# Performance work log

Measured on AMD Instinct MI355X. Metric: run time of the kernel, lower is better.

The kernel has to match this reference:

```python
import jax, jax.numpy as jnp
import numpy as np

T, H, NH, NKV, HD = 4096, 2048, 16, 2, 256
ROT = 64           # partial_rotary_factor 0.25 * head_dim 256
HALF = ROT // 2    # 32 == sum(mrope_section [11, 11, 10])
BASE = 10_000_000.0
EPS = 1e-6
SCALE = HD ** -0.5


def setup_inputs() -> dict:
    key = jax.random.key(0)
    ks = jax.random.split(key, 8)
    s = 0.02
    return {
        "positions": jnp.sort(jax.random.randint(ks[0], (3, T), 0, 4096), axis=-1),
        "hidden": jax.random.normal(ks[1], (T, H), jnp.float32),
        "Wq": jax.random.normal(ks[2], (H, NH * HD * 2), jnp.float32) * s,
        "Wk": jax.random.normal(ks[3], (H, NKV * HD), jnp.float32) * s,
        "Wv": jax.random.normal(ks[4], (H, NKV * HD), jnp.float32) * s,
        "Wo": jax.random.normal(ks[5], (NH * HD, H), jnp.float32) * s,
        "q_norm_w": jax.random.normal(ks[6], (HD,), jnp.float32) * 0.1,
        "k_norm_w": jax.random.normal(ks[7], (HD,), jnp.float32) * 0.1,
    }


def _rms(x, w):
    # GemmaRMSNorm: x / rms * (1 + w), per-head over last dim
    var = jnp.mean(x * x, axis=-1, keepdims=True)
    return x * jax.lax.rsqrt(var + EPS) * (1.0 + w)


def _rope_tables(positions):
    # interleaved MRoPE: freq j uses position axis j % 3 -> counts [11,11,10]
    inv_freq = BASE ** (-jnp.arange(0, ROT, 2, dtype=jnp.float32) / ROT)  # [HALF]
    axis = jnp.arange(HALF) % 3
    pos = positions[axis, :].astype(jnp.float32)   # [HALF, T]
    freqs = pos.T * inv_freq                       # [T, HALF]
    return jnp.cos(freqs), jnp.sin(freqs)


def _apply_rope(x, cos, sin):
    # x: [T, heads, HD]; rotate first ROT dims (neox half-split), rest pass through
    x1, x2 = x[..., :HALF], x[..., HALF:ROT]
    c, s = cos[:, None, :], sin[:, None, :]
    return jnp.concatenate([x1 * c - x2 * s, x2 * c + x1 * s, x[..., ROT:]], axis=-1)


def reference(positions, hidden, Wq, Wk, Wv, Wo, q_norm_w, k_norm_w):
    qg = (hidden @ Wq).reshape(T, NH, 2 * HD)
    q, gate = qg[..., :HD], qg[..., HD:]          # chunk(2, dim=-1)
    k = (hidden @ Wk).reshape(T, NKV, HD)
    v = (hidden @ Wv).reshape(T, NKV, HD)
    q = _rms(q, q_norm_w)
    k = _rms(k, k_norm_w)
    cos, sin = _rope_tables(positions)
    q = _apply_rope(q, cos, sin)
    k = _apply_rope(k, cos, sin)
    # GQA causal attention: group 16 Q heads over 2 KV heads
    g = NH // NKV
    q4 = q.reshape(T, NKV, g, HD)
    scores = jnp.einsum('qkgd,tkd->kgqt', q4, k) * SCALE   # [NKV, g, T, T]
    mask = jnp.tril(jnp.ones((T, T), dtype=bool))
    scores = jnp.where(mask[None, None], scores, -jnp.inf)
    probs = jax.nn.softmax(scores, axis=-1)
    o = jnp.einsum('kgqt,tkd->qkgd', probs, v).reshape(T, NH, HD)
    o = o * jax.nn.sigmoid(gate)                   # per-head output gating
    return o.reshape(T, NH * HD) @ Wo
```

## Files before the change

kernel.cpp:

```cpp
#include <hip/hip_runtime.h>
#include <hip/hip_bf16.h>


#define T_SZ 4096
#define H_SZ 2048
#define NH_SZ 16
#define NKV_SZ 2
#define HD_SZ 256
#define ATT_SCALE 0.0625f
#define SOFT_M 18.0f
#define EPS_ 1e-6f

typedef __attribute__((ext_vector_type(8))) short bf16x8;
typedef __attribute__((ext_vector_type(4))) float f32x4;

#define MFMA16(a, b, c) __builtin_amdgcn_mfma_f32_16x16x32_bf16((a), (b), (c), 0, 0, 0)

__device__ __forceinline__ void async16(const void* g, void* l) {
  __builtin_amdgcn_global_load_lds((const __attribute__((address_space(1))) void*)g,
                                   (__attribute__((address_space(3))) void*)l,
                                   16, 0, 0);
}

__device__ __forceinline__ float to_f(float x) { return x; }
__device__ __forceinline__ float to_f(__hip_bfloat16 x) { return __bfloat162float(x); }

union BfBits { __hip_bfloat16 h; unsigned short u; };

__device__ __forceinline__ unsigned short bf16_bits(__hip_bfloat16 h) {
  BfBits t; t.h = h; return t.u;
}

__device__ __forceinline__ unsigned pack_hilo(float v) {
  __hip_bfloat16 hi = __float2bfloat16(v);
  float rem = v - __bfloat162float(hi);
  __hip_bfloat16 lo = __float2bfloat16(rem);
  return (unsigned)bf16_bits(hi) | ((unsigned)bf16_bits(lo) << 16);
}

__global__ __launch_bounds__(256) void cast_f32_bf16(const float* __restrict__ in,
                                                     __hip_bfloat16* __restrict__ out,
                                                     int n4) {
  int i = blockIdx.x * 256 + threadIdx.x;
  if (i >= n4) return;
  float4 v = ((const float4*)in)[i];
  union { __hip_bfloat16 h[4]; uint2 u; } t;
  t.h[0] = __float2bfloat16(v.x);
  t.h[1] = __float2bfloat16(v.y);
  t.h[2] = __float2bfloat16(v.z);
  t.h[3] = __float2bfloat16(v.w);
  ((uint2*)out)[i] = t.u;
}

template <typename TIN>
__global__ __launch_bounds__(256) void transpose_cast(const TIN* __restrict__ in,
                                                      __hip_bfloat16* __restrict__ out,
                                                      int R, int C) {
  __shared__ TIN tile[32][33];
  int c0 = blockIdx.x * 32, r0 = blockIdx.y * 32;
  int tx = threadIdx.x & 31, ty = threadIdx.x >> 5;
#pragma unroll
  for (int i = 0; i < 32; i += 8)
    tile[ty + i][tx] = in[(long)(r0 + ty + i) * C + c0 + tx];
  __syncthreads();
#pragma unroll
  for (int i = 0; i < 32; i += 8)
    out[(long)(c0 + ty + i) * R + r0 + tx] = __float2bfloat16(to_f(tile[tx][ty + i]));
}

__global__ __launch_bounds__(512) void gemm_qg2(const __hip_bfloat16* __restrict__ A,
                                                const __hip_bfloat16* __restrict__ BT,
                                                float* __restrict__ qout,
                                                __hip_bfloat16* __restrict__ gate) {
  __shared__ __align__(16) __hip_bfloat16 As[4][8192];
  __shared__ __align__(16) __hip_bfloat16 Bs[4][8192];
  const int tid = threadIdx.x, wid = tid >> 6, lane = tid & 63;
  const int lo = lane & 15, quad = lane >> 4;
  const int wm = (wid >> 2) * 128, wn = (wid & 3) * 64;
  const int wg = blockIdx.x + blockIdx.y * 8;
  const int xcd = wg & 7, i_ = wg >> 3;
  const long n0 = (long)(xcd * 4 + (i_ & 3)) * 256;
  const long m0 = (long)(i_ >> 2) * 256;
  const int K = 2048;

  const int r0_ = tid >> 2;
  const int kc0 = (tid & 3) ^ ((tid >> 3) & 3);
  const __hip_bfloat16* sA0 = A + (m0 + r0_) * K + kc0 * 8;
  const __hip_bfloat16* sA1 = A + (m0 + r0_ + 128) * K + kc0 * 8;
  const __hip_bfloat16* sB0 = BT + (n0 + r0_) * K + kc0 * 8;
  const __hip_bfloat16* sB1 = BT + (n0 + r0_ + 128) * K + kc0 * 8;

  const int xq = (lo >> 1) & 3;
  const int aoff = (wm + lo) * 32 + ((quad ^ xq) * 8);
  const int boff = (wn + lo) * 32 + ((quad ^ xq) * 8);

  const f32x4 z4 = {0.f, 0.f, 0.f, 0.f};
  f32x4 acc[8][4];
#pragma unroll
  for (int fr = 0; fr < 8; ++fr)
#pragma unroll
    for (int fn = 0; fn < 4; ++fn) acc[fr][fn] = z4;

#define QG_STAGE(buf, kt) do {                                   \
    const int off_ = (kt) * 32;                                  \
    async16(sA0 + off_, &As[buf][tid * 8]);                      \
    async16(sA1 + off_, &As[buf][tid * 8 + 4096]);               \
    async16(sB0 + off_, &Bs[buf][tid * 8]);                      \
    async16(sB1 + off_, &Bs[buf][tid * 8 + 4096]);               \
  } while (0)

#define QG_COMPUTE(buf_) do {                                    \
    bf16x8 af[8], bq[4];                                         \
    _Pragma("unroll")                                            \
    for (int fr = 0; fr < 8; ++fr)                               \
      af[fr] = *(const bf16x8*)(&As[buf_][aoff + fr * 512]);     \
    _Pragma("unroll")                                            \
    for (int fn = 0; fn < 4; ++fn)                               \
      bq[fn] = *(const bf16x8*)(&Bs[buf_][boff + fn * 512]);     \
    __builtin_amdgcn_s_setprio(1);                               \
    _Pragma("unroll")                                            \
    for (int fr = 0; fr < 8; ++fr)                               \
      _Pragma("unroll")                                          \
      for (int fn = 0; fn < 4; ++fn)                             \
        acc[fr][fn] = MFMA16(af[fr], bq[fn], acc[fr][fn]);       \
    __builtin_amdgcn_s_setprio(0);                               \
  } while (0)

  QG_STAGE(0, 0); QG_STAGE(1, 1); QG_STAGE(2, 2);
  for (int kt = 0; kt < 61; ++kt) {
    asm volatile("s_waitcnt vmcnt(8)" ::: "memory");
    __builtin_amdgcn_s_barrier();
    __builtin_amdgcn_sched_barrier(0);
    QG_STAGE((kt + 3) & 3, kt + 3);
    __builtin_amdgcn_sched_barrier(0);
    QG_COMPUTE(kt & 3);
  }
  asm volatile("s_waitcnt vmcnt(8)" ::: "memory");
  __builtin_amdgcn_s_barrier();
  __builtin_amdgcn_sched_barrier(0);
  QG_COMPUTE(1);
  asm volatile("s_waitcnt vmcnt(4)" ::: "memory");
  __builtin_amdgcn_s_barrier();
  __builtin_amdgcn_sched_barrier(0);
  QG_COMPUTE(2);
  asm volatile("s_waitcnt vmcnt(0)" ::: "memory");
  __builtin_amdgcn_s_barrier();
  __builtin_amdgcn_sched_barrier(0);
  QG_COMPUTE(3);
#undef QG_STAGE
#undef QG_COMPUTE

#pragma unroll
  for (int fr = 0; fr < 8; ++fr)
#pragma unroll
    for (int fn = 0; fn < 4; ++fn)
#pragma unroll
      for (int rr = 0; rr < 4; ++rr) {
        long row = m0 + wm + fr * 16 + quad * 4 + rr;
        long col = n0 + wn + fn * 16 + lo;
        int head = (int)(col >> 9), c = (int)(col & 511);
        float v = acc[fr][fn][rr];
        if (c < 256)
          qout[(row * NH_SZ + head) * 256 + c] = v;
        else
          gate[(row * NH_SZ + head) * 256 + (c - 256)] = __float2bfloat16(v);
      }
}

__global__ __launch_bounds__(256) void gemm_kv(const __hip_bfloat16* __restrict__ A,
                                               const __hip_bfloat16* __restrict__ BT,
                                               float* __restrict__ kf,
                                               __hip_bfloat16* __restrict__ vraw,
                                               int M, int N, int K) {
  __shared__ __align__(16) __hip_bfloat16 As[128 * 32];
  __shared__ __align__(16) __hip_bfloat16 Bs[128 * 32];
  const int tid = threadIdx.x;
  const int wid = tid >> 6, lane = tid & 63;
  const int lo = lane & 15, quad = lane >> 4;
  const int wq = blockIdx.x + blockIdx.y * 8;
  const int xcd = wq & 7, idx = wq >> 3;
  const long n0 = (long)xcd * 128;
  const long m0 = (long)idx * 128;
  const int wm = (wid >> 1) * 64, wn = (wid & 1) * 64;
  const f32x4 z4 = {0.f, 0.f, 0.f, 0.f};
  f32x4 acc[4][4];
#pragma unroll
  for (int i = 0; i < 4; ++i)
#pragma unroll
    for (int j = 0; j < 4; ++j) acc[i][j] = z4;

  const int cf0 = tid, cf1 = 256 + tid;
  const int r0_ = cf0 >> 2, c0_ = (cf0 & 3) * 8;
  const int r1_ = cf1 >> 2, c1_ = (cf1 & 3) * 8;
  const __hip_bfloat16* a0 = A + (m0 + r0_) * K + c0_;
  const __hip_bfloat16* a1 = A + (m0 + r1_) * K + c1_;
  const __hip_bfloat16* b0 = BT + (n0 + r0_) * K + c0_;
  const __hip_bfloat16* b1 = BT + (n0 + r1_) * K + c1_;

  for (int k0 = 0; k0 < K; k0 += 32) {
    async16(a0 + k0, As + cf0 * 8);
    async16(a1 + k0, As + cf1 * 8);
    async16(b0 + k0, Bs + cf0 * 8);
    async16(b1 + k0, Bs + cf1 * 8);
    __syncthreads();
    bf16x8 af[4], bfv[4];
#pragma unroll
    for (int i = 0; i < 4; ++i)
      af[i] = *(const bf16x8*)(As + (wm + i * 16 + lo) * 32 + quad * 8);
#pragma unroll
    for (int i = 0; i < 4; ++i)
      bfv[i] = *(const bf16x8*)(Bs + (wn + i * 16 + lo) * 32 + quad * 8);
#pragma unroll
    for (int i = 0; i < 4; ++i)
#pragma unroll
      for (int j = 0; j < 4; ++j) acc[i][j] = MFMA16(af[i], bfv[j], acc[i][j]);
    __syncthreads();
  }
#pragma unroll
  for (int i = 0; i < 4; ++i)
#pragma unroll
    for (int j = 0; j < 4; ++j)
#pragma unroll
      for (int r = 0; r < 4; ++r) {
        long row = m0 + wm + i * 16 + quad * 4 + r;
        long col = n0 + wn + j * 16 + lo;
        float v = acc[i][j][r];
        if (col < 512)
          kf[row * 512 + col] = v;
        else
          vraw[row * 512 + (col - 512)] = __float2bfloat16(v);
      }
}

__global__ __launch_bounds__(256) void v_swizzle(const __hip_bfloat16* __restrict__ vraw,
                                                 __hip_bfloat16* __restrict__ vsw) {
  const int ktt = blockIdx.x, kvh = blockIdx.y, tid = threadIdx.x;
  __shared__ __hip_bfloat16 L[64 * 264];
#pragma unroll
  for (int it = 0; it < 8; ++it) {
    int cf = it * 256 + tid;
    int kv = cf >> 5, d0 = (cf & 31) * 8;
    *(uint4*)&L[kv * 264 + d0] =
        *(const uint4*)&vraw[(((long)ktt * 64 + kv) * NKV_SZ + kvh) * 256 + d0];
  }
  __syncthreads();
#pragma unroll
  for (int it = 0; it < 8; ++it) {
    int cf = it * 256 + tid;
    int c = cf >> 8, d = cf & 255;
    union { __hip_bfloat16 h[8]; uint4 u; } t;
#pragma unroll
    for (int e = 0; e < 8; ++e) t.h[e] = L[(c * 8 + e) * 264 + d];
    *(uint4*)&vsw[((long)kvh * 64 + ktt) * 16384 + (long)(c * 256 + d) * 8] = t.u;
  }
}

__global__ __launch_bounds__(256) void norm_rope_wave(float* __restrict__ qbuf,
                                                      const float* __restrict__ kbuf,
                                                      __hip_bfloat16* __restrict__ ksw,
                                                      const int* __restrict__ pos,
                                                      const float* __restrict__ qw,
                                                      const float* __restrict__ kw) {
  const int id = blockIdx.x * 4 + (threadIdx.x >> 6);
  const int lane = threadIdx.x & 63;
  const int h = id % 18, t = id / 18;
  const bool isq = h < NH_SZ;
  const float* ptr = isq ? qbuf + ((long)t * NH_SZ + h) * 256
                         : kbuf + ((long)t * NKV_SZ + (h - NH_SZ)) * 256;
  const float* w = isq ? qw : kw;
  float4 v = *(const float4*)(ptr + lane * 4);
  float4 wv = *(const float4*)(w + lane * 4);
  float s2 = v.x * v.x + v.y * v.y + v.z * v.z + v.w * v.w;
#pragma unroll
  for (int o = 32; o > 0; o >>= 1) s2 += __shfl_xor(s2, o);
  float sc = rsqrtf(s2 * (1.0f / 256.0f) + EPS_);
  float n[4];
  n[0] = v.x * sc * (1.0f + wv.x);
  n[1] = v.y * sc * (1.0f + wv.y);
  n[2] = v.z * sc * (1.0f + wv.z);
  n[3] = v.w * sc * (1.0f + wv.w);
  float pr[4];
#pragma unroll
  for (int j = 0; j < 4; ++j) pr[j] = __shfl_xor(n[j], 8);
  float o4[4];
  if (lane < 16) {
    int base_i = (lane & 7) * 4;
#pragma unroll
    for (int j = 0; j < 4; ++j) {
      int i = base_i + j;
      float p = (float)pos[(i % 3) * T_SZ + t];
      float fr = p * exp2f((float)i * (-0.72667177075661f));
      float c, s;
      sincosf(fr, &s, &c);
      o4[j] = (lane < 8) ? n[j] * c - pr[j] * s : n[j] * c + pr[j] * s;
    }
  } else {
#pragma unroll
    for (int j = 0; j < 4; ++j) o4[j] = n[j];
  }
  if (isq) {
    uint4 u;
    u.x = pack_hilo(o4[0]); u.y = pack_hilo(o4[1]);
    u.z = pack_hilo(o4[2]); u.w = pack_hilo(o4[3]);
    *(uint4*)((unsigned*)qbuf + ((long)t * NH_SZ + h) * 256 + lane * 4) = u;
  } else {
    int kv = h - NH_SZ;
    long tt = t >> 5; int r = t & 31;
    int c = lane >> 1, e0 = (lane & 1) * 4;
    union { __hip_bfloat16 h4[4]; uint2 u; } kk;
#pragma unroll
    for (int j = 0; j < 4; ++j) kk.h4[j] = __float2bfloat16(o4[j]);
    *(uint2*)&ksw[(((long)kv * 128 + tt) * 32 + c) * 256 + r * 8 + e0] = kk.u;
  }
}

__global__ __launch_bounds__(256) void attn_kernel(unsigned* __restrict__ Qp,
                                                   const __hip_bfloat16* __restrict__ Ksw,
                                                   const __hip_bfloat16* __restrict__ Vsw,
                                                   const __hip_bfloat16* __restrict__ Gt) {
  const int w = blockIdx.x + blockIdx.y * 64;
  const int xcd = w & 7, j = w >> 3;
  const int h = xcd * 2 + (j & 1);
  const int qt = 63 - (j >> 1);
  const int kvh = h >> 3;
  const int tid = threadIdx.x, wid = tid >> 6, lane = tid & 63;
  const int lo = lane & 15, quad = lane >> 4;
  __shared__ __align__(16) __hip_bfloat16 Ks[32 * 256];
  __shared__ __align__(16) __hip_bfloat16 Vs[4 * 2048];
  __shared__ __align__(16) __hip_bfloat16 Ps[4][16 * 40];

  __hip_bfloat16* myP = &Ps[wid][0];
  const f32x4 z4 = {0.f, 0.f, 0.f, 0.f};
  const int nt = 2 * (qt + 1);

  bf16x8 qh[8], ql[8];
  {
    const unsigned* qp =
        Qp + ((long)(qt * 64 + wid * 16 + lo) * NH_SZ + h) * 256 + quad * 8;
#pragma unroll
    for (int kc = 0; kc < 8; ++kc) {
      uint4 p0 = *(const uint4*)(qp + kc * 32);
      uint4 p1 = *(const uint4*)(qp + kc * 32 + 4);
      bf16x8 a, b;
      a[0] = (short)(p0.x & 0xffff); b[0] = (short)(p0.x >> 16);
      a[1] = (short)(p0.y & 0xffff); b[1] = (short)(p0.y >> 16);
      a[2] = (short)(p0.z & 0xffff); b[2] = (short)(p0.z >> 16);
      a[3] = (short)(p0.w & 0xffff); b[3] = (short)(p0.w >> 16);
      a[4] = (short)(p1.x & 0xffff); b[4] = (short)(p1.x >> 16);
      a[5] = (short)(p1.y & 0xffff); b[5] = (short)(p1.y >> 16);
      a[6] = (short)(p1.z & 0xffff); b[6] = (short)(p1.z >> 16);
      a[7] = (short)(p1.w & 0xffff); b[7] = (short)(p1.w >> 16);
      qh[kc] = a; ql[kc] = b;
    }
  }

  f32x4 acc[16];
#pragma unroll
  for (int od = 0; od < 16; ++od) acc[od] = z4;
  float lsum[4];
#pragma unroll
  for (int r = 0; r < 4; ++r) lsum[r] = 0.f;

  const int qrow_g = qt * 64 + wid * 16 + quad * 4;
  const __hip_bfloat16* kbase = Ksw + (long)kvh * 1048576;
  const __hip_bfloat16* vbase = Vsw + (long)kvh * 1048576;

#pragma unroll
  for (int i = 0; i < 4; ++i) {
    int m = i * 4 + wid;
    async16(kbase + m * 512 + lane * 8, Ks + m * 512 + lane * 8);
    async16(vbase + m * 512 + lane * 8, Vs + m * 512 + lane * 8);
  }
  __syncthreads();

  for (int kt = 0; kt < nt; ++kt) {
    const bool skip = (kt == nt - 1) && (wid < 2);
    f32x4 s[2];
    s[0] = z4; s[1] = z4;
    if (!skip) {
      __builtin_amdgcn_s_setprio(1);
#pragma unroll
      for (int kc = 0; kc < 8; ++kc) {
        bf16x8 ah = qh[kc], al = ql[kc];
#pragma unroll
        for (int ni = 0; ni < 2; ++ni) {
          bf16x8 b = *(const bf16x8*)(Ks + (kc * 4 + quad) * 256 + (ni * 16 + lo) * 8);
          s[ni] = MFMA16(ah, b, s[ni]);
          s[ni] = MFMA16(al, b, s[ni]);
        }
      }
      __builtin_amdgcn_s_setprio(0);
    }
    __syncthreads();
    if (kt + 1 < nt) {
      const __hip_bfloat16* kb = kbase + (long)(kt + 1) * 8192;
#pragma unroll
      for (int i = 0; i < 4; ++i) {
        int m = i * 4 + wid;
        async16(kb + m * 512 + lane * 8, Ks + m * 512 + lane * 8);
      }
    }
    if (!skip) {
      float sv[2][4];
      if (kt >= nt - 2) {
#pragma unroll
        for (int ni = 0; ni < 2; ++ni) {
          int kcol = kt * 32 + ni * 16 + lo;
#pragma unroll
          for (int r = 0; r < 4; ++r) {
            float e = __expf(fmaf(s[ni][r], ATT_SCALE, -SOFT_M));
            sv[ni][r] = (kcol > qrow_g + r) ? 0.f : e;
          }
        }
      } else {
#pragma unroll
        for (int ni = 0; ni < 2; ++ni)
#pragma unroll
          for (int r = 0; r < 4; ++r)
            sv[ni][r] = __expf(fmaf(s[ni][r], ATT_SCALE, -SOFT_M));
      }
#pragma unroll
      for (int r = 0; r < 4; ++r) lsum[r] += sv[0][r] + sv[1][r];
#pragma unroll
      for (int ni = 0; ni < 2; ++ni)
#pragma unroll
        for (int r = 0; r < 4; ++r)
          myP[(quad * 4 + r) * 40 + ni * 16 + lo] = __float2bfloat16(sv[ni][r]);
      bf16x8 ap = *(const bf16x8*)(myP + lo * 40 + quad * 8);
      __builtin_amdgcn_s_setprio(1);
#pragma unroll
      for (int od = 0; od < 16; ++od) {
        bf16x8 bv = *(const bf16x8*)(Vs + quad * 2048 + (od * 16 + lo) * 8);
        acc[od] = MFMA16(ap, bv, acc[od]);
      }
      __builtin_amdgcn_s_setprio(0);
    }
    __syncthreads();
    if (kt + 1 < nt) {
      const __hip_bfloat16* vb = vbase + (long)(kt + 1) * 8192;
#pragma unroll
      for (int i = 0; i < 4; ++i) {
        int m = i * 4 + wid;
        async16(vb + m * 512 + lane * 8, Vs + m * 512 + lane * 8);
      }
    }
  }

  float l_r[4];
#pragma unroll
  for (int r = 0; r < 4; ++r) {
    float su = lsum[r];
#pragma unroll
    for (int off = 1; off < 16; off <<= 1) su += __shfl_xor(su, off);
    l_r[r] = su;
  }
#pragma unroll
  for (int od = 0; od < 16; ++od)
#pragma unroll
    for (int r = 0; r < 4; ++r) {
      int trow = qt * 64 + wid * 16 + quad * 4 + r;
      int col = od * 16 + lo;
      long idx = ((long)trow * NH_SZ + h) * 256 + col;
      float g = __bfloat162float(Gt[idx]);
      float sig = 1.0f / (1.0f + expf(-g));
      float v = (acc[od][r] / l_r[r]) * sig;
      Qp[idx] = pack_hilo(v);
    }
}

__global__ __launch_bounds__(256) void gemm_out(const unsigned* __restrict__ Ap,
                                                const __hip_bfloat16* __restrict__ Bt,
                                                float* __restrict__ C,
                                                int M, int N, int K) {
  __shared__ __align__(16) __hip_bfloat16 Ash[128 * 32];
  __shared__ __align__(16) __hip_bfloat16 Asl[128 * 32];
  __shared__ __align__(16) __hip_bfloat16 Bs[128 * 32];
  const int tid = threadIdx.x;
  const int wid = tid >> 6, lane = tid & 63;
  const int lo = lane & 15, quad = lane >> 4;
  const int wq = blockIdx.x + blockIdx.y * 16;
  const int xcd = wq & 7, idx = wq >> 3;
  const long n0 = (long)(xcd * 2 + (idx & 1)) * 128;
  const long m0 = (long)(idx >> 1) * 128;
  const int wm = (wid >> 1) * 64, wn = (wid & 1) * 64;
  const f32x4 z4 = {0.f, 0.f, 0.f, 0.f};
  f32x4 acc[4][4];
#pragma unroll
  for (int i = 0; i < 4; ++i)
#pragma unroll
    for (int j = 0; j < 4; ++j) acc[i][j] = z4;

  const int cf0 = tid, cf1 = 256 + tid;
  const int br0 = cf0 >> 2, bc0 = (cf0 & 3) * 8;
  const int br1 = cf1 >> 2, bc1 = (cf1 & 3) * 8;
  const __hip_bfloat16* b0 = Bt + (n0 + br0) * K + bc0;
  const __hip_bfloat16* b1 = Bt + (n0 + br1) * K + bc1;

  for (int k0 = 0; k0 < K; k0 += 32) {
    async16(b0 + k0, Bs + cf0 * 8);
    async16(b1 + k0, Bs + cf1 * 8);
#pragma unroll
    for (int it = 0; it < 4; ++it) {
      int c = it * 256 + tid, row = c >> 3, c4 = (c & 7) * 4;
      uint4 p = *(const uint4*)(Ap + (m0 + row) * K + k0 + c4);
      uint2 wh, wl;
      wh.x = (p.x & 0xffff) | ((p.y & 0xffff) << 16);
      wh.y = (p.z & 0xffff) | ((p.w & 0xffff) << 16);
      wl.x = (p.x >> 16) | (p.y & 0xffff0000u);
      wl.y = (p.z >> 16) | (p.w & 0xffff0000u);
      *(uint2*)(Ash + row * 32 + c4) = wh;
      *(uint2*)(Asl + row * 32 + c4) = wl;
    }
    __syncthreads();
    bf16x8 ah[4], al[4], bf[4];
#pragma unroll
    for (int i = 0; i < 4; ++i) {
      ah[i] = *(const bf16x8*)(Ash + (wm + i * 16 + lo) * 32 + quad * 8);
      al[i] = *(const bf16x8*)(Asl + (wm + i * 16 + lo) * 32 + quad * 8);
      bf[i] = *(const bf16x8*)(Bs + (wn + i * 16 + lo) * 32 + quad * 8);
    }
#pragma unroll
    for (int i = 0; i < 4; ++i)
#pragma unroll
      for (int j = 0; j < 4; ++j) {
        acc[i][j] = MFMA16(ah[i], bf[j], acc[i][j]);
        acc[i][j] = MFMA16(al[i], bf[j], acc[i][j]);
      }
    __syncthreads();
  }
#pragma unroll
  for (int i = 0; i < 4; ++i)
#pragma unroll
    for (int j = 0; j < 4; ++j)
#pragma unroll
      for (int r = 0; r < 4; ++r) {
        long row = m0 + wm + i * 16 + quad * 4 + r;
        long col = n0 + wn + j * 16 + lo;
        C[row * N + col] = acc[i][j][r];
      }
}

extern "C" void kernel_launch(void* const* d_in, const int* in_sizes, int n_in,
                              void* d_out, int out_size, void* d_ws, size_t ws_size,
                              hipStream_t stream) {
  (void)in_sizes; (void)n_in; (void)out_size; (void)ws_size;
  const int* positions = (const int*)d_in[0];
  const float* hidden = (const float*)d_in[1];
  const float* Wq = (const float*)d_in[2];
  const float* Wk = (const float*)d_in[3];
  const float* Wv = (const float*)d_in[4];
  const float* Wo = (const float*)d_in[5];
  const float* qw = (const float*)d_in[6];
  const float* kw = (const float*)d_in[7];
  float* out = (float*)d_out;
  char* ws = (char*)d_ws;

  __hip_bfloat16* hid  = (__hip_bfloat16*)(ws + 0);
  __hip_bfloat16* WqT  = (__hip_bfloat16*)(ws + 16777216);
  __hip_bfloat16* WkT  = (__hip_bfloat16*)(ws + 50331648);
  __hip_bfloat16* WvT  = (__hip_bfloat16*)(ws + 52428800);
  float*          qf   = (float*)(ws + 54525952);
  __hip_bfloat16* gate = (__hip_bfloat16*)(ws + 121634816);
  float*          kf   = (float*)(ws + 155189248);
  __hip_bfloat16* vraw = (__hip_bfloat16*)(ws + 163577856);
  __hip_bfloat16* Ksw  = WkT;
  __hip_bfloat16* Vsw  = hid;
  __hip_bfloat16* WoT  = gate;
  unsigned* qpk = (unsigned*)qf;

  cast_f32_bf16<<<dim3(8192), dim3(256), 0, stream>>>(hidden, hid, 2097152);
  transpose_cast<float><<<dim3(256, 64), dim3(256), 0, stream>>>(Wq, WqT, 2048, 8192);
  transpose_cast<float><<<dim3(16, 64), dim3(256), 0, stream>>>(Wk, WkT, 2048, 512);
  transpose_cast<float><<<dim3(16, 64), dim3(256), 0, stream>>>(Wv, WvT, 2048, 512);
  gemm_qg2<<<dim3(8, 64), dim3(512), 0, stream>>>(hid, WqT, qf, gate);
  gemm_kv<<<dim3(8, 32), dim3(256), 0, stream>>>(hid, WkT, kf, vraw, 4096, 1024, 2048);
  v_swizzle<<<dim3(64, 2), dim3(256), 0, stream>>>(vraw, Vsw);
  norm_rope_wave<<<dim3(18432), dim3(256), 0, stream>>>(qf, kf, Ksw, positions, qw, kw);
  attn_kernel<<<dim3(64, 16), dim3(256), 0, stream>>>(qpk, Ksw, Vsw, gate);
  transpose_cast<float><<<dim3(64, 128), dim3(256), 0, stream>>>(Wo, WoT, 4096, 2048);
  gemm_out<<<dim3(16, 32), dim3(256), 0, stream>>>(qpk, WoT, out, 4096, 2048, 4096);
}
```

Before: 802.3 us.

## Rewrite output GEMM with async 4-stage pipeline over packed hi/lo activations

Replaces the output projection GEMM with a 512-thread, 256x128-tile kernel that streams A and B into LDS through a 4-deep async global_load_lds pipeline with XOR swizzle and raised MFMA priority. Instead of splitting the packed hi/lo bf16 activations in registers, it treats the packed array as an interleaved K=8192 bf16 matrix and duplicates each Wo weight into both halves, so one MFMA chain computes hi*w + lo*w. This removes the per-iteration register unpacking and synchronous staging but doubles the Wo bytes written by the transpose and read by the GEMM.

```diff
diff --git a/kernel.cpp b/kernel.cpp
--- a/kernel.cpp
+++ b/kernel.cpp
@@ -66,6 +66,23 @@
 #pragma unroll
   for (int i = 0; i < 32; i += 8)
     out[(long)(c0 + ty + i) * R + r0 + tx] = __float2bfloat16(to_f(tile[tx][ty + i]));
+}
+
+__global__ __launch_bounds__(256) void transpose_dup(const float* __restrict__ in,
+                                                     unsigned* __restrict__ out,
+                                                     int R, int C) {
+  __shared__ float tile[32][33];
+  int c0 = blockIdx.x * 32, r0 = blockIdx.y * 32;
+  int tx = threadIdx.x & 31, ty = threadIdx.x >> 5;
+#pragma unroll
+  for (int i = 0; i < 32; i += 8)
+    tile[ty + i][tx] = in[(long)(r0 + ty + i) * C + c0 + tx];
+  __syncthreads();
+#pragma unroll
+  for (int i = 0; i < 32; i += 8) {
+    unsigned short b = bf16_bits(__float2bfloat16(tile[tx][ty + i]));
+    out[(long)(c0 + ty + i) * R + r0 + tx] = (unsigned)b | ((unsigned)b << 16);
+  }
 }
 
 __global__ __launch_bounds__(512) void gemm_qg2(const __hip_bfloat16* __restrict__ A,
@@ -164,6 +181,96 @@
           qout[(row * NH_SZ + head) * 256 + c] = v;
         else
           gate[(row * NH_SZ + head) * 256 + (c - 256)] = __float2bfloat16(v);
+      }
+}
+
+__global__ __launch_bounds__(512) void gemm_out2(const __hip_bfloat16* __restrict__ A,
+                                                 const __hip_bfloat16* __restrict__ BT,
+                                                 float* __restrict__ C) {
+  __shared__ __align__(16) __hip_bfloat16 As[4][8192];
+  __shared__ __align__(16) __hip_bfloat16 Bs[4][4096];
+  const int tid = threadIdx.x, wid = tid >> 6, lane = tid & 63;
+  const int lo = lane & 15, quad = lane >> 4;
+  const int wm = (wid >> 1) * 64, wn = (wid & 1) * 64;
+  const int wg = blockIdx.x + blockIdx.y * 8;
+  const int xcd = wg & 7, i_ = wg >> 3;
+  const long n0 = (long)(xcd * 2 + (i_ & 1)) * 128;
+  const long m0 = (long)(i_ >> 1) * 256;
+  const long Kp = 8192;
+
+  const int rA = tid >> 2, spx = (tid & 3) ^ ((tid >> 2) & 3);
+  const __hip_bfloat16* sA0 = A + (m0 + rA) * Kp + spx * 8;
+  const __hip_bfloat16* sA1 = A + (m0 + rA + 128) * Kp + spx * 8;
+  const __hip_bfloat16* sB0 = BT + (n0 + rA) * Kp + spx * 8;
+
+  const int xa = quad ^ (lo & 3);
+  const int aoff = (wm + lo) * 32 + xa * 8;
+  const int boff = (wn + lo) * 32 + xa * 8;
+
+  const f32x4 z4 = {0.f, 0.f, 0.f, 0.f};
+  f32x4 acc[4][4];
+#pragma unroll
+  for (int fr = 0; fr < 4; ++fr)
+#pragma unroll
+    for (int fn = 0; fn < 4; ++fn) acc[fr][fn] = z4;
+
+#define GO_STAGE(buf, kt) do {                                   \
+    const long off_ = (long)(kt) * 32;                           \
+    async16(sA0 + off_, &As[buf][tid * 8]);                      \
+    async16(sA1 + off_, &As[buf][tid * 8 + 4096]);               \
+    async16(sB0 + off_, &Bs[buf][tid * 8]);                      \
+  } while (0)
+
+#define GO_COMPUTE(buf_) do {                                    \
+    bf16x8 af[4], bq[4];                                         \
+    _Pragma("unroll")                                            \
+    for (int fr = 0; fr < 4; ++fr)                               \
+      af[fr] = *(const bf16x8*)(&As[buf_][aoff + fr * 512]);     \
+    _Pragma("unroll")                                            \
+    for (int fn = 0; fn < 4; ++fn)                               \
+      bq[fn] = *(const bf16x8*)(&Bs[buf_][boff + fn * 512]);     \
+    __builtin_amdgcn_s_setprio(1);                               \
+    _Pragma("unroll")                                            \
+    for (int fr = 0; fr < 4; ++fr)                               \
+      _Pragma("unroll")                                          \
+      for (int fn = 0; fn < 4; ++fn)                             \
+        acc[fr][fn] = MFMA16(af[fr], bq[fn], acc[fr][fn]);       \
+    __builtin_amdgcn_s_setprio(0);                               \
+  } while (0)
+
+  GO_STAGE(0, 0); GO_STAGE(1, 1); GO_STAGE(2, 2);
+  for (int kt = 0; kt < 253; ++kt) {
+    asm volatile("s_waitcnt vmcnt(6)" ::: "memory");
+    __builtin_amdgcn_s_barrier();
+    __builtin_amdgcn_sched_barrier(0);
+    GO_STAGE((kt + 3) & 3, kt + 3);
+    __builtin_amdgcn_sched_barrier(0);
+    GO_COMPUTE(kt & 3);
+  }
+  asm volatile("s_waitcnt vmcnt(6)" ::: "memory");
+  __builtin_amdgcn_s_barrier();
+  __builtin_amdgcn_sched_barrier(0);
+  GO_COMPUTE(1);
+  asm volatile("s_waitcnt vmcnt(3)" ::: "memory");
+  __builtin_amdgcn_s_barrier();
+  __builtin_amdgcn_sched_barrier(0);
+  GO_COMPUTE(2);
+  asm volatile("s_waitcnt vmcnt(0)" ::: "memory");
+  __builtin_amdgcn_s_barrier();
+  __builtin_amdgcn_sched_barrier(0);
+  GO_COMPUTE(3);
+#undef GO_STAGE
+#undef GO_COMPUTE
+
+#pragma unroll
+  for (int fr = 0; fr < 4; ++fr)
+#pragma unroll
+    for (int fn = 0; fn < 4; ++fn)
+#pragma unroll
+      for (int rr = 0; rr < 4; ++rr) {
+        long row = m0 + wm + fr * 16 + quad * 4 + rr;
+        long col = n0 + wn + fn * 16 + lo;
+        C[row * 2048 + col] = acc[fr][fn][rr];
       }
 }
 
@@ -468,78 +575,6 @@
     }
 }
 
-__global__ __launch_bounds__(256) void gemm_out(const unsigned* __restrict__ Ap,
-                                                const __hip_bfloat16* __restrict__ Bt,
-                                                float* __restrict__ C,
-                                                int M, int N, int K) {
-  __shared__ __align__(16) __hip_bfloat16 Ash[128 * 32];
-  __shared__ __align__(16) __hip_bfloat16 Asl[128 * 32];
-  __shared__ __align__(16) __hip_bfloat16 Bs[128 * 32];
-  const int tid = threadIdx.x;
-  const int wid = tid >> 6, lane = tid & 63;
-  const int lo = lane & 15, quad = lane >> 4;
-  const int wq = blockIdx.x + blockIdx.y * 16;
-  const int xcd = wq & 7, idx = wq >> 3;
-  const long n0 = (long)(xcd * 2 + (idx & 1)) * 128;
-  const long m0 = (long)(idx >> 1) * 128;
-  const int wm = (wid >> 1) * 64, wn = (wid & 1) * 64;
-  const f32x4 z4 = {0.f, 0.f, 0.f, 0.f};
-  f32x4 acc[4][4];
-#pragma unroll
-  for (int i = 0; i < 4; ++i)
-#pragma unroll
-    for (int j = 0; j < 4; ++j) acc[i][j] = z4;
-
-  const int cf0 = tid, cf1 = 256 + tid;
-  const int br0 = cf0 >> 2, bc0 = (cf0 & 3) * 8;
-  const int br1 = cf1 >> 2, bc1 = (cf1 & 3) * 8;
-  const __hip_bfloat16* b0 = Bt + (n0 + br0) * K + bc0;
-  const __hip_bfloat16* b1 = Bt + (n0 + br1) * K + bc1;
-
-  for (int k0 = 0; k0 < K; k0 += 32) {
-    async16(b0 + k0, Bs + cf0 * 8);
-    async16(b1 + k0, Bs + cf1 * 8);
-#pragma unroll
-    for (int it = 0; it < 4; ++it) {
-      int c = it * 256 + tid, row = c >> 3, c4 = (c & 7) * 4;
-      uint4 p = *(const uint4*)(Ap + (m0 + row) * K + k0 + c4);
-      uint2 wh, wl;
-      wh.x = (p.x & 0xffff) | ((p.y & 0xffff) << 16);
-      wh.y = (p.z & 0xffff) | ((p.w & 0xffff) << 16);
-      wl.x = (p.x >> 16) | (p.y & 0xffff0000u);
-      wl.y = (p.z >> 16) | (p.w & 0xffff0000u);
-      *(uint2*)(Ash + row * 32 + c4) = wh;
-      *(uint2*)(Asl + row * 32 + c4) = wl;
-    }
-    __syncthreads();
-    bf16x8 ah[4], al[4], bf[4];
-#pragma unroll
-    for (int i = 0; i < 4; ++i) {
-      ah[i] = *(const bf16x8*)(Ash + (wm + i * 16 + lo) * 32 + quad * 8);
-      al[i] = *(const bf16x8*)(Asl + (wm + i * 16 + lo) * 32 + quad * 8);
-      bf[i] = *(const bf16x8*)(Bs + (wn + i * 16 + lo) * 32 + quad * 8);
-    }
-#pragma unroll
-    for (int i = 0; i < 4; ++i)
-#pragma unroll
-      for (int j = 0; j < 4; ++j) {
-        acc[i][j] = MFMA16(ah[i], bf[j], acc[i][j]);
-        acc[i][j] = MFMA16(al[i], bf[j], acc[i][j]);
-      }
-    __syncthreads();
-  }
-#pragma unroll
-  for (int i = 0; i < 4; ++i)
-#pragma unroll
-    for (int j = 0; j < 4; ++j)
-#pragma unroll
-      for (int r = 0; r < 4; ++r) {
-        long row = m0 + wm + i * 16 + quad * 4 + r;
-        long col = n0 + wn + j * 16 + lo;
-        C[row * N + col] = acc[i][j][r];
-      }
-}
-
 extern "C" void kernel_launch(void* const* d_in, const int* in_sizes, int n_in,
                               void* d_out, int out_size, void* d_ws, size_t ws_size,
                               hipStream_t stream) {
@@ -565,7 +600,7 @@
   __hip_bfloat16* vraw = (__hip_bfloat16*)(ws + 163577856);
   __hip_bfloat16* Ksw  = WkT;
   __hip_bfloat16* Vsw  = hid;
-  __hip_bfloat16* WoT  = gate;
+  unsigned*       Wo2  = (unsigned*)WqT;
   unsigned* qpk = (unsigned*)qf;
 
   cast_f32_bf16<<<dim3(8192), dim3(256), 0, stream>>>(hidden, hid, 2097152);
@@ -577,6 +612,7 @@
   v_swizzle<<<dim3(64, 2), dim3(256), 0, stream>>>(vraw, Vsw);
   norm_rope_wave<<<dim3(18432), dim3(256), 0, stream>>>(qf, kf, Ksw, positions, qw, kw);
   attn_kernel<<<dim3(64, 16), dim3(256), 0, stream>>>(qpk, Ksw, Vsw, gate);
-  transpose_cast<float><<<dim3(64, 128), dim3(256), 0, stream>>>(Wo, WoT, 4096, 2048);
-  gemm_out<<<dim3(16, 32), dim3(256), 0, stream>>>(qpk, WoT, out, 4096, 2048, 4096);
-}
+  transpose_dup<<<dim3(64, 128), dim3(256), 0, stream>>>(Wo, Wo2, 4096, 2048);
+  gemm_out2<<<dim3(8, 32), dim3(512), 0, stream>>>((const __hip_bfloat16*)qpk,
+                                                   (const __hip_bfloat16*)Wo2, out);
+}
```

After: 861.9 us. 7.4% more time.

## Fuse Q RMSNorm and RoPE into QG GEMM epilogue

Applied to the files above, without the earlier changes.

The Q/gate GEMM epilogue now computes the per-head RMS norm through a cross-wave LDS reduction, applies partial RoPE, and writes the packed hi/lo Q directly. This removes the fp32 Q round trip through global memory. The standalone norm kernel now processes only K heads. In exchange, the GEMM epilogue gains extra syncs, shuffles and sincos work.

```diff
diff --git a/kernel.cpp b/kernel.cpp
--- a/kernel.cpp
+++ b/kernel.cpp
@@ -70,13 +70,16 @@
 
 __global__ __launch_bounds__(512) void gemm_qg2(const __hip_bfloat16* __restrict__ A,
                                                 const __hip_bfloat16* __restrict__ BT,
-                                                float* __restrict__ qout,
-                                                __hip_bfloat16* __restrict__ gate) {
+                                                unsigned* __restrict__ qpk,
+                                                __hip_bfloat16* __restrict__ gate,
+                                                const int* __restrict__ pos,
+                                                const float* __restrict__ qw) {
   __shared__ __align__(16) __hip_bfloat16 As[4][8192];
   __shared__ __align__(16) __hip_bfloat16 Bs[4][8192];
   const int tid = threadIdx.x, wid = tid >> 6, lane = tid & 63;
   const int lo = lane & 15, quad = lane >> 4;
   const int wm = (wid >> 2) * 128, wn = (wid & 3) * 64;
+  const int wnx = wid & 3;
   const int wg = blockIdx.x + blockIdx.y * 8;
   const int xcd = wg & 7, i_ = wg >> 3;
   const long n0 = (long)(xcd * 4 + (i_ & 3)) * 256;
@@ -150,21 +153,67 @@
 #undef QG_STAGE
 #undef QG_COMPUTE
 
-#pragma unroll
-  for (int fr = 0; fr < 8; ++fr)
-#pragma unroll
-    for (int fn = 0; fn < 4; ++fn)
+  const int head = (int)(n0 >> 9);
+  const bool isq = ((n0 >> 8) & 1) == 0;
+  if (!isq) {
+#pragma unroll
+    for (int fr = 0; fr < 8; ++fr)
+#pragma unroll
+      for (int fn = 0; fn < 4; ++fn)
+#pragma unroll
+        for (int rr = 0; rr < 4; ++rr) {
+          long row = m0 + wm + fr * 16 + quad * 4 + rr;
+          int c = wn + fn * 16 + lo;
+          gate[(row * NH_SZ + head) * 256 + c] = __float2bfloat16(acc[fr][fn][rr]);
+        }
+  } else {
+    __syncthreads();
+    float* red = (float*)&As[0][0];
+#pragma unroll
+    for (int fr = 0; fr < 8; ++fr)
 #pragma unroll
       for (int rr = 0; rr < 4; ++rr) {
-        long row = m0 + wm + fr * 16 + quad * 4 + rr;
-        long col = n0 + wn + fn * 16 + lo;
-        int head = (int)(col >> 9), c = (int)(col & 511);
-        float v = acc[fr][fn][rr];
-        if (c < 256)
-          qout[(row * NH_SZ + head) * 256 + c] = v;
-        else
-          gate[(row * NH_SZ + head) * 256 + (c - 256)] = __float2bfloat16(v);
-      }
+        float p = 0.f;
+#pragma unroll
+        for (int fn = 0; fn < 4; ++fn) { float x = acc[fr][fn][rr]; p += x * x; }
+#pragma unroll
+        for (int off = 1; off < 16; off <<= 1) p += __shfl_xor(p, off);
+        if (lo == 0) red[(wm + fr * 16 + quad * 4 + rr) * 4 + wnx] = p;
+      }
+    __syncthreads();
+    float wq4[4];
+#pragma unroll
+    for (int fn = 0; fn < 4; ++fn) wq4[fn] = 1.0f + qw[wn + fn * 16 + lo];
+#pragma unroll
+    for (int fr = 0; fr < 8; ++fr)
+#pragma unroll
+      for (int rr = 0; rr < 4; ++rr) {
+        int rl = wm + fr * 16 + quad * 4 + rr;
+        float4 rv = *(const float4*)&red[rl * 4];
+        float sc = rsqrtf((rv.x + rv.y + rv.z + rv.w) * (1.0f / 256.0f) + EPS_);
+        float v[4];
+#pragma unroll
+        for (int fn = 0; fn < 4; ++fn) v[fn] = acc[fr][fn][rr] * sc * wq4[fn];
+        long row = m0 + rl;
+        if (wnx == 0) {
+#pragma unroll
+          for (int fnp = 0; fnp < 2; ++fnp) {
+            int i = fnp * 16 + lo;
+            float p = (float)pos[(i % 3) * T_SZ + row];
+            float fr_ = p * exp2f((float)i * (-0.72667177075661f));
+            float cc, ss;
+            sincosf(fr_, &ss, &cc);
+            float x1 = v[fnp], x2 = v[fnp + 2];
+            v[fnp] = x1 * cc - x2 * ss;
+            v[fnp + 2] = x2 * cc + x1 * ss;
+          }
+        }
+        long base = (row * NH_SZ + head) * 256;
+#pragma unroll
+        for (int fn = 0; fn < 4; ++fn)
+          qpk[base + wn + fn * 16 + lo] = pack_hilo(v[fn]);
+      }
+  }
 }
 
 __global__ __launch_bounds__(256) void gemm_kv(const __hip_bfloat16* __restrict__ A,
@@ -255,21 +304,16 @@
   }
 }
 
-__global__ __launch_bounds__(256) void norm_rope_wave(float* __restrict__ qbuf,
-                                                      const float* __restrict__ kbuf,
-                                                      __hip_bfloat16* __restrict__ ksw,
-                                                      const int* __restrict__ pos,
-                                                      const float* __restrict__ qw,
-                                                      const float* __restrict__ kw) {
+__global__ __launch_bounds__(256) void norm_rope_k(const float* __restrict__ kbuf,
+                                                   __hip_bfloat16* __restrict__ ksw,
+                                                   const int* __restrict__ pos,
+                                                   const float* __restrict__ kw) {
   const int id = blockIdx.x * 4 + (threadIdx.x >> 6);
   const int lane = threadIdx.x & 63;
-  const int h = id % 18, t = id / 18;
-  const bool isq = h < NH_SZ;
-  const float* ptr = isq ? qbuf + ((long)t * NH_SZ + h) * 256
-                         : kbuf + ((long)t * NKV_SZ + (h - NH_SZ)) * 256;
-  const float* w = isq ? qw : kw;
+  const int kv = id & 1, t = id >> 1;
+  const float* ptr = kbuf + ((long)t * NKV_SZ + kv) * 256;
   float4 v = *(const float4*)(ptr + lane * 4);
-  float4 wv = *(const float4*)(w + lane * 4);
+  float4 wv = *(const float4*)(kw + lane * 4);
   float s2 = v.x * v.x + v.y * v.y + v.z * v.z + v.w * v.w;
 #pragma unroll
   for (int o = 32; o > 0; o >>= 1) s2 += __shfl_xor(s2, o);
@@ -298,20 +342,12 @@
 #pragma unroll
     for (int j = 0; j < 4; ++j) o4[j] = n[j];
   }
-  if (isq) {
-    uint4 u;
-    u.x = pack_hilo(o4[0]); u.y = pack_hilo(o4[1]);
-    u.z = pack_hilo(o4[2]); u.w = pack_hilo(o4[3]);
-    *(uint4*)((unsigned*)qbuf + ((long)t * NH_SZ + h) * 256 + lane * 4) = u;
-  } else {
-    int kv = h - NH_SZ;
-    long tt = t >> 5; int r = t & 31;
-    int c = lane >> 1, e0 = (lane & 1) * 4;
-    union { __hip_bfloat16 h4[4]; uint2 u; } kk;
-#pragma unroll
-    for (int j = 0; j < 4; ++j) kk.h4[j] = __float2bfloat16(o4[j]);
-    *(uint2*)&ksw[(((long)kv * 128 + tt) * 32 + c) * 256 + r * 8 + e0] = kk.u;
-  }
+  long tt = t >> 5; int r = t & 31;
+  int c = lane >> 1, e0 = (lane & 1) * 4;
+  union { __hip_bfloat16 h4[4]; uint2 u; } kk;
+#pragma unroll
+  for (int j = 0; j < 4; ++j) kk.h4[j] = __float2bfloat16(o4[j]);
+  *(uint2*)&ksw[(((long)kv * 128 + tt) * 32 + c) * 256 + r * 8 + e0] = kk.u;
 }
 
 __global__ __launch_bounds__(256) void attn_kernel(unsigned* __restrict__ Qp,
@@ -572,10 +608,10 @@
   transpose_cast<float><<<dim3(256, 64), dim3(256), 0, stream>>>(Wq, WqT, 2048, 8192);
   transpose_cast<float><<<dim3(16, 64), dim3(256), 0, stream>>>(Wk, WkT, 2048, 512);
   transpose_cast<float><<<dim3(16, 64), dim3(256), 0, stream>>>(Wv, WvT, 2048, 512);
-  gemm_qg2<<<dim3(8, 64), dim3(512), 0, stream>>>(hid, WqT, qf, gate);
+  gemm_qg2<<<dim3(8, 64), dim3(512), 0, stream>>>(hid, WqT, qpk, gate, positions, qw);
   gemm_kv<<<dim3(8, 32), dim3(256), 0, stream>>>(hid, WkT, kf, vraw, 4096, 1024, 2048);
   v_swizzle<<<dim3(64, 2), dim3(256), 0, stream>>>(vraw, Vsw);
-  norm_rope_wave<<<dim3(18432), dim3(256), 0, stream>>>(qf, kf, Ksw, positions, qw, kw);
+  norm_rope_k<<<dim3(2048), dim3(256), 0, stream>>>(kf, Ksw, positions, kw);
   attn_kernel<<<dim3(64, 16), dim3(256), 0, stream>>>(qpk, Ksw, Vsw, gate);
   transpose_cast<float><<<dim3(64, 128), dim3(256), 0, stream>>>(Wo, WoT, 4096, 2048);
   gemm_out<<<dim3(16, 32), dim3(256), 0, stream>>>(qpk, WoT, out, 4096, 2048, 4096);
```

Result: slower. 826.3 us (+3.0%).
